# Performance work log

Measured on AMD Instinct MI355X. Metric: run time of the kernel, lower is better.

## Reference

```python
import jax, jax.numpy as jnp
import numpy as np

C = 1024          # columns
K = 16            # cells per column
S = 32            # distal segments per cell
Y = 128           # synapses per segment
N = C * K         # num cells
PERM_THR = 0.5
ACT_THR = 10
LR = 0.1          # volatile learning rate
MOD = 1.0         # modulation_signal


def setup_inputs() -> dict:
    key = jax.random.key(0)
    k1, k2, k3, k4, k5 = jax.random.split(key, 5)
    x = jax.random.uniform(k1, (C,)) < 0.03                      # sparse column SDR
    prev_active_cells = jax.random.uniform(k2, (N,)) < 0.12      # prev-step active cells
    distal_connections = jax.random.randint(k3, (N, S, Y), 0, N, dtype=jnp.int32)
    volatile_permanences = jax.random.uniform(k4, (N, S, Y), dtype=jnp.float32)
    consolidated_permanences = jax.random.uniform(k5, (N, S, Y), dtype=jnp.float32) * 0.6
    return {
        "x": x,
        "prev_active_cells": prev_active_cells,
        "distal_connections": distal_connections,
        "volatile_permanences": volatile_permanences,
        "consolidated_permanences": consolidated_permanences,
    }


def reference(x, prev_active_cells, distal_connections, volatile_permanences, consolidated_permanences):
    conn = jnp.clip(distal_connections, 0, N - 1)                # [N,S,Y]
    x_active = x.astype(bool)                                    # [C]
    prev_any = prev_active_cells.any()

    # ---- phase 1: predictive state per column from prev_active_cells ----
    presyn_prev = prev_active_cells[conn]                        # [N,S,Y] irregular gather
    connected = (volatile_permanences > PERM_THR) | (consolidated_permanences > PERM_THR)
    active_syn = (connected & presyn_prev).sum(-1)               # [N,S]
    pred_cell = (active_syn >= ACT_THR).any(-1)                  # [N]
    pred_col = pred_cell.reshape(C, K)                           # [C,K]
    col_predicted = pred_col.any(-1)                             # [C]

    # ---- burst winner selection (unthresholded overlaps, argmax over K*S) ----
    overlaps = presyn_prev.sum(-1).astype(jnp.int32)             # [N,S]
    best_flat = jnp.argmax(overlaps.reshape(C, K * S), axis=-1)  # [C]
    burst_winner_local = best_flat // S                          # [C] (== 0 when no prev activity, matching torch fallback)
    burst_winner_mask = jax.nn.one_hot(burst_winner_local, K, dtype=bool)  # [C,K]

    winner = jnp.where(col_predicted[:, None], pred_col, burst_winner_mask)  # [C,K]
    winner = winner & x_active[:, None]                          # only active columns

    # new active cells: only bursting columns set cells (predicted columns set none, per source)
    new_active = jnp.broadcast_to((x_active & ~col_predicted)[:, None], (C, K))
    new_active_flat = new_active.reshape(-1)                     # [N]

    # ---- learning: update volatile permanences on each winner cell's best segment ----
    best_seg = jnp.argmax(overlaps, axis=-1)                     # [N]
    rows = jnp.arange(N)
    presyn_best = presyn_prev[rows, best_seg]                    # [N,Y]
    old_row = volatile_permanences[rows, best_seg]               # [N,Y]
    pot = LR * MOD
    pun = pot * 0.1
    new_row = jnp.clip(old_row + jnp.where(presyn_best, pot, -pun), 0.0, 1.0)
    learn_mask = winner.reshape(-1) & prev_any                   # [N] (torch skips learning if no prev activity)
    vol_new = volatile_permanences.at[rows, best_seg].set(
        jnp.where(learn_mask[:, None], new_row, old_row))

    # ---- phase 2: predictive state for next step from new active cells + updated perms ----
    presyn_new = new_active_flat[conn]                           # [N,S,Y]
    connected2 = (vol_new > PERM_THR) | (consolidated_permanences > PERM_THR)
    pred_next = (((connected2 & presyn_new).sum(-1)) >= ACT_THR).any(-1)  # [N]

    num_active = x_active.sum()
    num_pred = (x_active & col_predicted).sum()
    acc = jnp.where(num_active > 0,
                    num_pred.astype(jnp.float32) / jnp.maximum(num_active, 1).astype(jnp.float32),
                    jnp.float32(1.0))
    return new_active_flat, pred_next, acc
```

## Files before the change

kernel.cpp:

```cpp
#include <hip/hip_runtime.h>
#include <stdint.h>

#define C_ 1024
#define K_ 16
#define S_ 32
#define Y_ 128
#define N_ (C_ * K_)
#define ACT_THR 10
#define PERM_THR 0.5f
#define POT 0.1f
#define PUN 0.01f

#define WS_NUM_ACTIVE 0
#define WS_NUM_PRED   1
#define WS_NBURST     2
#define WS_LEARN_CNT  3
#define WS_PREV_ANY   4
#define WS_BURSTMASK  8
#define WS_PREVMASK   64
#define WS_CELLINFO   1024
#define WS_LIST       (1024 + N_)
#define WS_CONBITS    65536


__global__ __launch_bounds__(512) void pack_kernel(const int* __restrict__ prev,
                                                   unsigned* __restrict__ ws) {
    const int tid = threadIdx.x;
    if (tid < 64) ws[tid] = 0u;
    __syncthreads();
    const int4* p = reinterpret_cast<const int4*>(prev + tid * 32);
    unsigned m = 0u;
    #pragma unroll
    for (int q = 0; q < 8; ++q) {
        const int4 v = p[q];
        m |= (v.x != 0 ? 1u : 0u) << (q * 4 + 0);
        m |= (v.y != 0 ? 1u : 0u) << (q * 4 + 1);
        m |= (v.z != 0 ? 1u : 0u) << (q * 4 + 2);
        m |= (v.w != 0 ? 1u : 0u) << (q * 4 + 3);
    }
    ws[WS_PREVMASK + tid] = m;
    const bool any = (__ballot(m != 0u) != 0ull);
    if ((tid & 63) == 0 && any) atomicOr(&ws[WS_PREV_ANY], 1u);
}

__global__ __launch_bounds__(256) void precompute_kernel(const float* __restrict__ vol,
                                                         const float* __restrict__ cons,
                                                         unsigned long long* __restrict__ conbits) {
    const int tid  = threadIdx.x;
    const int wave = tid >> 6;
    const int lane = tid & 63;
    const int half = lane >> 5;
    const int l32  = lane & 31;
    const int cell = blockIdx.x * 4 + wave;
    const size_t base = (size_t)cell * (S_ * Y_) + (size_t)half * Y_ + (size_t)(l32 * 4);

    float4 v0 = *reinterpret_cast<const float4*>(vol  + base);
    float4 s0 = *reinterpret_cast<const float4*>(cons + base);
    float4 v1 = *reinterpret_cast<const float4*>(vol  + base + 256);
    float4 s1 = *reinterpret_cast<const float4*>(cons + base + 256);

    unsigned long long bits = 0ull;
    #pragma unroll 4
    for (int i = 0; i < 16; ++i) {
        const float4 vv = v0, sv = s0;
        v0 = v1; s0 = s1;
        if (i < 14) {
            const size_t nb = base + (size_t)(i + 2) * 256;
            v1 = *reinterpret_cast<const float4*>(vol  + nb);
            s1 = *reinterpret_cast<const float4*>(cons + nb);
        }
        const unsigned nib = ((vv.x > PERM_THR || sv.x > PERM_THR) ? 1u : 0u)
                           | ((vv.y > PERM_THR || sv.y > PERM_THR) ? 2u : 0u)
                           | ((vv.z > PERM_THR || sv.z > PERM_THR) ? 4u : 0u)
                           | ((vv.w > PERM_THR || sv.w > PERM_THR) ? 8u : 0u);
        bits |= ((unsigned long long)nib) << (4 * i);
    }
    conbits[(size_t)cell * 64 + lane] = bits;
}

__global__ __launch_bounds__(256) void phase1b_kernel(const int* __restrict__ conn,
                                                      const unsigned long long* __restrict__ conbits,
                                                      unsigned* __restrict__ ws) {
    __shared__ unsigned prevmask[512];
    const int tid = threadIdx.x;
    for (int i = tid; i < 512; i += 256) prevmask[i] = ws[WS_PREVMASK + i];
    __syncthreads();

    const int wave = tid >> 6;
    const int lane = tid & 63;
    const int half = lane >> 5;
    const int l32  = lane & 31;
    const int sh   = half * 32;
    const int cell = blockIdx.x * 4 + wave;
    const size_t base = (size_t)cell * (S_ * Y_) + (size_t)half * Y_ + (size_t)(l32 * 4);

    unsigned long long bits = conbits[(size_t)cell * 64 + lane];
    int4 a0 = *reinterpret_cast<const int4*>(conn + base);
    int4 a1 = *reinterpret_cast<const int4*>(conn + base + 256);

    unsigned key = 0u;
    bool predf = false;

    #pragma unroll 4
    for (int i = 0; i < 16; ++i) {
        const int4 cv = a0;
        a0 = a1;
        if (i < 14) a1 = *reinterpret_cast<const int4*>(conn + base + (size_t)(i + 2) * 256);

        const unsigned nib = (unsigned)bits & 0xFu;
        bits >>= 4;

        const int m0 = min(max(cv.x, 0), N_ - 1);
        const int m1 = min(max(cv.y, 0), N_ - 1);
        const int m2 = min(max(cv.z, 0), N_ - 1);
        const int m3 = min(max(cv.w, 0), N_ - 1);
        const bool p0 = (prevmask[m0 >> 5] >> (m0 & 31)) & 1u;
        const bool p1 = (prevmask[m1 >> 5] >> (m1 & 31)) & 1u;
        const bool p2 = (prevmask[m2 >> 5] >> (m2 & 31)) & 1u;
        const bool p3 = (prevmask[m3 >> 5] >> (m3 & 31)) & 1u;
        const bool c0 = nib & 1u;
        const bool c1 = nib & 2u;
        const bool c2 = nib & 4u;
        const bool c3 = nib & 8u;

        const uint64_t bp0 = __ballot(p0), bp1 = __ballot(p1),
                       bp2 = __ballot(p2), bp3 = __ballot(p3);
        const uint64_t ba0 = __ballot(p0 && c0), ba1 = __ballot(p1 && c1),
                       ba2 = __ballot(p2 && c2), ba3 = __ballot(p3 && c3);

        const int ov = __popc((unsigned)(bp0 >> sh)) + __popc((unsigned)(bp1 >> sh)) +
                       __popc((unsigned)(bp2 >> sh)) + __popc((unsigned)(bp3 >> sh));
        const int ac = __popc((unsigned)(ba0 >> sh)) + __popc((unsigned)(ba1 >> sh)) +
                       __popc((unsigned)(ba2 >> sh)) + __popc((unsigned)(ba3 >> sh));

        predf |= (ac >= ACT_THR);
        const int seg = 2 * i + half;
        const unsigned k2 = ((unsigned)ov << 6) | (unsigned)(63 - seg);
        key = max(key, k2);
    }

    const unsigned okey = (unsigned)__shfl_xor((int)key, 32);
    const unsigned fkey = max(key, okey);
    const bool fpred = (__any(predf ? 1 : 0) != 0);
    if (lane == 0) {
        const int bo = (int)(fkey >> 6);
        const int bs = 63 - (int)(fkey & 63u);
        ws[WS_CELLINFO + cell] = (fpred ? 1u : 0u) | ((unsigned)bs << 8) | ((unsigned)bo << 16);
    }
}

__global__ __launch_bounds__(256) void column_kernel(const int* __restrict__ x,
                                                     unsigned*  __restrict__ ws,
                                                     float*     __restrict__ out_new_active) {
    const int c = blockIdx.x * 256 + threadIdx.x;
    if (c >= C_) return;
    const bool xa = (x[c] != 0);
    const int base = c * K_;

    unsigned info[K_];
    bool colpred = false;
    int bo = -1, bk = 0;
    #pragma unroll
    for (int k = 0; k < K_; ++k) {
        const unsigned inf = ws[WS_CELLINFO + base + k];
        info[k] = inf;
        if (inf & 1u) colpred = true;
        const int ov = (int)((inf >> 16) & 0xFFu);
        if (ov > bo) { bo = ov; bk = k; }
    }

    const bool burst = xa && !colpred;
    const float nav = burst ? 1.0f : 0.0f;
    #pragma unroll
    for (int k = 0; k < K_; ++k) out_new_active[base + k] = nav;

    if (xa) {
        atomicAdd(&ws[WS_NUM_ACTIVE], 1u);
        if (colpred) atomicAdd(&ws[WS_NUM_PRED], 1u);
    }
    if (burst) {
        atomicAdd(&ws[WS_NBURST], 1u);
        atomicOr(&ws[WS_BURSTMASK + (c >> 5)], 1u << (c & 31));
    }
    if (xa) {
        if (colpred) {
            #pragma unroll
            for (int k = 0; k < K_; ++k) {
                if (info[k] & 1u) {
                    const unsigned i = atomicAdd(&ws[WS_LEARN_CNT], 1u);
                    ws[WS_LIST + i] = (unsigned)(base + k);
                }
            }
        } else {
            const unsigned i = atomicAdd(&ws[WS_LEARN_CNT], 1u);
            ws[WS_LIST + i] = (unsigned)(base + bk);
        }
    }
}

__global__ __launch_bounds__(256) void learnb_kernel(const int*   __restrict__ conn,
                                                     float*       __restrict__ vol,
                                                     const float* __restrict__ cons,
                                                     unsigned*    __restrict__ ws,
                                                     float*       __restrict__ out_acc) {
    __shared__ unsigned prevmask[512];
    const int tid = threadIdx.x;
    for (int i = tid; i < 512; i += 256) prevmask[i] = ws[WS_PREVMASK + i];
    __syncthreads();

    if (blockIdx.x == 0 && tid == 0) {
        const int na  = (int)ws[WS_NUM_ACTIVE];
        const int np_ = (int)ws[WS_NUM_PRED];
        out_acc[0] = (na > 0) ? ((float)np_ / (float)na) : 1.0f;
    }
    if (ws[WS_PREV_ANY] == 0u) return;

    const int cnt = (int)ws[WS_LEARN_CNT];
    const int hw  = (blockIdx.x * 256 + tid) >> 5;
    const int g   = tid & 31;
    const int nhw = gridDim.x * 8;
    unsigned* conbits32 = ws + WS_CONBITS;

    for (int e = hw; e < cnt; e += nhw) {
        const int cellv = (int)ws[WS_LIST + e];
        const int seg   = (int)((ws[WS_CELLINFO + cellv] >> 8) & 0xFFu);
        const size_t base = ((size_t)cellv * S_ + seg) * Y_ + (size_t)(g * 4);
        const int4   cv = *reinterpret_cast<const int4*>(conn + base);
        float4       vv = *reinterpret_cast<float4*>(vol + base);
        const float4 sv = *reinterpret_cast<const float4*>(cons + base);
        const int m0 = min(max(cv.x, 0), N_ - 1);
        const int m1 = min(max(cv.y, 0), N_ - 1);
        const int m2 = min(max(cv.z, 0), N_ - 1);
        const int m3 = min(max(cv.w, 0), N_ - 1);
        const bool p0 = (prevmask[m0 >> 5] >> (m0 & 31)) & 1u;
        const bool p1 = (prevmask[m1 >> 5] >> (m1 & 31)) & 1u;
        const bool p2 = (prevmask[m2 >> 5] >> (m2 & 31)) & 1u;
        const bool p3 = (prevmask[m3 >> 5] >> (m3 & 31)) & 1u;
        vv.x = fminf(fmaxf(vv.x + (p0 ? POT : -PUN), 0.0f), 1.0f);
        vv.y = fminf(fmaxf(vv.y + (p1 ? POT : -PUN), 0.0f), 1.0f);
        vv.z = fminf(fmaxf(vv.z + (p2 ? POT : -PUN), 0.0f), 1.0f);
        vv.w = fminf(fmaxf(vv.w + (p3 ? POT : -PUN), 0.0f), 1.0f);
        *reinterpret_cast<float4*>(vol + base) = vv;

        const unsigned nib = ((vv.x > PERM_THR || sv.x > PERM_THR) ? 1u : 0u)
                           | ((vv.y > PERM_THR || sv.y > PERM_THR) ? 2u : 0u)
                           | ((vv.z > PERM_THR || sv.z > PERM_THR) ? 4u : 0u)
                           | ((vv.w > PERM_THR || sv.w > PERM_THR) ? 8u : 0u);
        const int chunk = seg >> 1;
        const int slot  = (seg & 1) * 32 + g;
        const unsigned idx = (unsigned)(cellv * 128 + slot * 2 + (chunk >> 3));
        const int shn = 4 * (chunk & 7);
        const unsigned old = conbits32[idx];
        conbits32[idx] = (old & ~(0xFu << shn)) | (nib << shn);
    }
}

__global__ __launch_bounds__(256) void phase2b_kernel(const int* __restrict__ conn,
                                                      const unsigned long long* __restrict__ conbits,
                                                      const unsigned* __restrict__ ws,
                                                      float* __restrict__ out_pred_next) {
    __shared__ unsigned nburst_s;
    __shared__ unsigned burstmask[32];
    const int tid = threadIdx.x;
    if (tid == 0) nburst_s = ws[WS_NBURST];
    if (tid >= 64 && tid < 96) burstmask[tid - 64] = ws[WS_BURSTMASK + (tid - 64)];
    __syncthreads();

    const int cbase = blockIdx.x * 4;
    if (nburst_s == 0u) {
        if (tid < 4) out_pred_next[cbase + tid] = 0.0f;
        return;
    }

    const int wave = tid >> 6;
    const int lane = tid & 63;
    const int half = lane >> 5;
    const int l32  = lane & 31;
    const int sh   = half * 32;
    const int cell = cbase + wave;
    const size_t base = (size_t)cell * (S_ * Y_) + (size_t)half * Y_ + (size_t)(l32 * 4);

    unsigned long long bits = conbits[(size_t)cell * 64 + lane];
    int4 a0 = *reinterpret_cast<const int4*>(conn + base);
    int4 a1 = *reinterpret_cast<const int4*>(conn + base + 256);

    bool predf = false;

    #pragma unroll 4
    for (int i = 0; i < 16; ++i) {
        const int4 cv = a0;
        a0 = a1;
        if (i < 14) a1 = *reinterpret_cast<const int4*>(conn + base + (size_t)(i + 2) * 256);

        const unsigned nib = (unsigned)bits & 0xFu;
        bits >>= 4;

        const int m0 = min(max(cv.x, 0), N_ - 1) >> 4;
        const int m1 = min(max(cv.y, 0), N_ - 1) >> 4;
        const int m2 = min(max(cv.z, 0), N_ - 1) >> 4;
        const int m3 = min(max(cv.w, 0), N_ - 1) >> 4;
        const bool p0 = (burstmask[m0 >> 5] >> (m0 & 31)) & 1u;
        const bool p1 = (burstmask[m1 >> 5] >> (m1 & 31)) & 1u;
        const bool p2 = (burstmask[m2 >> 5] >> (m2 & 31)) & 1u;
        const bool p3 = (burstmask[m3 >> 5] >> (m3 & 31)) & 1u;
        const bool c0 = nib & 1u;
        const bool c1 = nib & 2u;
        const bool c2 = nib & 4u;
        const bool c3 = nib & 8u;

        const uint64_t ba0 = __ballot(p0 && c0), ba1 = __ballot(p1 && c1),
                       ba2 = __ballot(p2 && c2), ba3 = __ballot(p3 && c3);
        const int ac = __popc((unsigned)(ba0 >> sh)) + __popc((unsigned)(ba1 >> sh)) +
                       __popc((unsigned)(ba2 >> sh)) + __popc((unsigned)(ba3 >> sh));
        predf |= (ac >= ACT_THR);
    }

    const bool fpred = (__any(predf ? 1 : 0) != 0);
    if (lane == 0) out_pred_next[cell] = fpred ? 1.0f : 0.0f;
}

__global__ __launch_bounds__(256) void phase1_old(const int*   __restrict__ conn,
                                                  const float* __restrict__ vol,
                                                  const float* __restrict__ cons,
                                                  unsigned*    __restrict__ ws) {
    __shared__ unsigned prevmask[512];
    const int tid = threadIdx.x;
    for (int i = tid; i < 512; i += 256) prevmask[i] = ws[WS_PREVMASK + i];
    __syncthreads();

    const int wave = tid >> 6;
    const int lane = tid & 63;
    const int half = lane >> 5;
    const int l32  = lane & 31;
    const int sh   = half * 32;

    #pragma unroll 1
    for (int ci = 0; ci < 2; ++ci) {
        const int cell = blockIdx.x * 8 + wave + ci * 4;
        const size_t cellbase = (size_t)cell * (S_ * Y_) + (size_t)(l32 * 4);

        size_t a = cellbase + (size_t)half * Y_;
        int4   cv_n = *reinterpret_cast<const int4*>(conn + a);
        float4 vv_n = *reinterpret_cast<const float4*>(vol + a);
        float4 sv_n = *reinterpret_cast<const float4*>(cons + a);

        unsigned key = 0u;
        bool predf = false;

        #pragma unroll 2
        for (int i = 0; i < 16; ++i) {
            const int4   cv = cv_n;
            const float4 vv = vv_n;
            const float4 sv = sv_n;
            if (i < 15) {
                const size_t nb = cellbase + (size_t)(2 * (i + 1) + half) * Y_;
                cv_n = *reinterpret_cast<const int4*>(conn + nb);
                vv_n = *reinterpret_cast<const float4*>(vol + nb);
                sv_n = *reinterpret_cast<const float4*>(cons + nb);
            }

            const int m0 = min(max(cv.x, 0), N_ - 1);
            const int m1 = min(max(cv.y, 0), N_ - 1);
            const int m2 = min(max(cv.z, 0), N_ - 1);
            const int m3 = min(max(cv.w, 0), N_ - 1);
            const bool p0 = (prevmask[m0 >> 5] >> (m0 & 31)) & 1u;
            const bool p1 = (prevmask[m1 >> 5] >> (m1 & 31)) & 1u;
            const bool p2 = (prevmask[m2 >> 5] >> (m2 & 31)) & 1u;
            const bool p3 = (prevmask[m3 >> 5] >> (m3 & 31)) & 1u;
            const bool c0 = (vv.x > PERM_THR) || (sv.x > PERM_THR);
            const bool c1 = (vv.y > PERM_THR) || (sv.y > PERM_THR);
            const bool c2 = (vv.z > PERM_THR) || (sv.z > PERM_THR);
            const bool c3 = (vv.w > PERM_THR) || (sv.w > PERM_THR);

            const uint64_t bp0 = __ballot(p0), bp1 = __ballot(p1),
                           bp2 = __ballot(p2), bp3 = __ballot(p3);
            const uint64_t ba0 = __ballot(p0 && c0), ba1 = __ballot(p1 && c1),
                           ba2 = __ballot(p2 && c2), ba3 = __ballot(p3 && c3);

            const int ov = __popc((unsigned)(bp0 >> sh)) + __popc((unsigned)(bp1 >> sh)) +
                           __popc((unsigned)(bp2 >> sh)) + __popc((unsigned)(bp3 >> sh));
            const int ac = __popc((unsigned)(ba0 >> sh)) + __popc((unsigned)(ba1 >> sh)) +
                           __popc((unsigned)(ba2 >> sh)) + __popc((unsigned)(ba3 >> sh));

            predf |= (ac >= ACT_THR);
            const int seg = 2 * i + half;
            const unsigned k2 = ((unsigned)ov << 6) | (unsigned)(63 - seg);
            key = max(key, k2);
        }

        const unsigned okey = (unsigned)__shfl_xor((int)key, 32);
        const unsigned fkey = max(key, okey);
        const bool fpred = (__any(predf ? 1 : 0) != 0);
        if (lane == 0) {
            const int bo = (int)(fkey >> 6);
            const int bs = 63 - (int)(fkey & 63u);
            ws[WS_CELLINFO + cell] = (fpred ? 1u : 0u) | ((unsigned)bs << 8) | ((unsigned)bo << 16);
        }
    }
}

__global__ __launch_bounds__(256) void learn_old(const int* __restrict__ conn,
                                                 float*     __restrict__ vol,
                                                 unsigned*  __restrict__ ws,
                                                 float*     __restrict__ out_acc) {
    __shared__ unsigned prevmask[512];
    const int tid = threadIdx.x;
    for (int i = tid; i < 512; i += 256) prevmask[i] = ws[WS_PREVMASK + i];
    __syncthreads();

    if (blockIdx.x == 0 && tid == 0) {
        const int na  = (int)ws[WS_NUM_ACTIVE];
        const int np_ = (int)ws[WS_NUM_PRED];
        out_acc[0] = (na > 0) ? ((float)np_ / (float)na) : 1.0f;
    }
    if (ws[WS_PREV_ANY] == 0u) return;

    const int cnt    = (int)ws[WS_LEARN_CNT];
    const int wave   = (blockIdx.x * 256 + tid) >> 6;
    const int lane   = tid & 63;
    const int nwaves = gridDim.x * 4;

    for (int e = wave; e < cnt; e += nwaves) {
        const int cell = (int)ws[WS_LIST + e];
        const int seg  = (int)((ws[WS_CELLINFO + cell] >> 8) & 0xFFu);
        const size_t base = ((size_t)cell * S_ + seg) * Y_ + (size_t)(lane * 2);
        const int2 cv = *reinterpret_cast<const int2*>(conn + base);
        float2 vv = *reinterpret_cast<const float2*>(vol + base);
        const int m0 = min(max(cv.x, 0), N_ - 1);
        const int m1 = min(max(cv.y, 0), N_ - 1);
        const bool p0 = (prevmask[m0 >> 5] >> (m0 & 31)) & 1u;
        const bool p1 = (prevmask[m1 >> 5] >> (m1 & 31)) & 1u;
        vv.x = fminf(fmaxf(vv.x + (p0 ? POT : -PUN), 0.0f), 1.0f);
        vv.y = fminf(fmaxf(vv.y + (p1 ? POT : -PUN), 0.0f), 1.0f);
        *reinterpret_cast<float2*>(vol + base) = vv;
    }
}

__global__ __launch_bounds__(256) void phase2_old(const int*   __restrict__ conn,
                                                  const float* __restrict__ vol,
                                                  const float* __restrict__ cons,
                                                  const unsigned* __restrict__ ws,
                                                  float* __restrict__ out_pred_next) {
    __shared__ unsigned nburst_s;
    __shared__ unsigned burstmask[32];
    const int tid = threadIdx.x;
    if (tid == 0) nburst_s = ws[WS_NBURST];
    if (tid >= 64 && tid < 96) burstmask[tid - 64] = ws[WS_BURSTMASK + (tid - 64)];
    __syncthreads();

    const int cbase = blockIdx.x * 8;
    if (nburst_s == 0u) {
        if (tid < 8) out_pred_next[cbase + tid] = 0.0f;
        return;
    }

    const int wave = tid >> 6;
    const int lane = tid & 63;
    const int half = lane >> 5;
    const int l32  = lane & 31;
    const int sh   = half * 32;

    #pragma unroll 1
    for (int ci = 0; ci < 2; ++ci) {
        const int cell = cbase + wave + ci * 4;
        const size_t cellbase = (size_t)cell * (S_ * Y_) + (size_t)(l32 * 4);

        size_t a = cellbase + (size_t)half * Y_;
        int4   cv_n = *reinterpret_cast<const int4*>(conn + a);
        float4 vv_n = *reinterpret_cast<const float4*>(vol + a);
        float4 sv_n = *reinterpret_cast<const float4*>(cons + a);

        bool predf = false;

        #pragma unroll 2
        for (int i = 0; i < 16; ++i) {
            const int4   cv = cv_n;
            const float4 vv = vv_n;
            const float4 sv = sv_n;
            if (i < 15) {
                const size_t nb = cellbase + (size_t)(2 * (i + 1) + half) * Y_;
                cv_n = *reinterpret_cast<const int4*>(conn + nb);
                vv_n = *reinterpret_cast<const float4*>(vol + nb);
                sv_n = *reinterpret_cast<const float4*>(cons + nb);
            }

            const int m0 = min(max(cv.x, 0), N_ - 1) >> 4;
            const int m1 = min(max(cv.y, 0), N_ - 1) >> 4;
            const int m2 = min(max(cv.z, 0), N_ - 1) >> 4;
            const int m3 = min(max(cv.w, 0), N_ - 1) >> 4;
            const bool p0 = (burstmask[m0 >> 5] >> (m0 & 31)) & 1u;
            const bool p1 = (burstmask[m1 >> 5] >> (m1 & 31)) & 1u;
            const bool p2 = (burstmask[m2 >> 5] >> (m2 & 31)) & 1u;
            const bool p3 = (burstmask[m3 >> 5] >> (m3 & 31)) & 1u;
            const bool c0 = (vv.x > PERM_THR) || (sv.x > PERM_THR);
            const bool c1 = (vv.y > PERM_THR) || (sv.y > PERM_THR);
            const bool c2 = (vv.z > PERM_THR) || (sv.z > PERM_THR);
            const bool c3 = (vv.w > PERM_THR) || (sv.w > PERM_THR);

            const uint64_t ba0 = __ballot(p0 && c0), ba1 = __ballot(p1 && c1),
                           ba2 = __ballot(p2 && c2), ba3 = __ballot(p3 && c3);
            const int ac = __popc((unsigned)(ba0 >> sh)) + __popc((unsigned)(ba1 >> sh)) +
                           __popc((unsigned)(ba2 >> sh)) + __popc((unsigned)(ba3 >> sh));
            predf |= (ac >= ACT_THR);
        }

        const bool fpred = (__any(predf ? 1 : 0) != 0);
        if (lane == 0) out_pred_next[cell] = fpred ? 1.0f : 0.0f;
    }
}

extern "C" void kernel_launch(void* const* d_in, const int* in_sizes, int n_in,
                              void* d_out, int out_size, void* d_ws, size_t ws_size,
                              hipStream_t stream) {
    const int*   x    = (const int*)d_in[0];
    const int*   prev = (const int*)d_in[1];
    const int*   conn = (const int*)d_in[2];
    float*       vol  = (float*)d_in[3];
    const float* cons = (const float*)d_in[4];
    float*    out = (float*)d_out;
    unsigned* ws  = (unsigned*)d_ws;

    const size_t need = (size_t)WS_CONBITS * 4 + (size_t)N_ * 64 * 8;

    pack_kernel<<<1, 512, 0, stream>>>(prev, ws);

    if (ws_size >= need) {
        unsigned long long* conbits = (unsigned long long*)(ws + WS_CONBITS);
        precompute_kernel<<<N_ / 4, 256, 0, stream>>>(vol, cons, conbits);
        phase1b_kernel   <<<N_ / 4, 256, 0, stream>>>(conn, conbits, ws);
        column_kernel    <<<C_ / 256, 256, 0, stream>>>(x, ws, out);
        learnb_kernel    <<<64, 256, 0, stream>>>(conn, vol, cons, ws, out + 2 * N_);
        phase2b_kernel   <<<N_ / 4, 256, 0, stream>>>(conn, conbits, ws, out + N_);
    } else {
        phase1_old<<<2048, 256, 0, stream>>>(conn, vol, cons, ws);
        column_kernel<<<C_ / 256, 256, 0, stream>>>(x, ws, out);
        learn_old<<<64, 256, 0, stream>>>(conn, vol, ws, out + 2 * N_);
        phase2_old<<<2048, 256, 0, stream>>>(conn, vol, cons, ws, out + N_);
    }
}
```

Before: 680.6 us.

## Fuse connectivity precompute into phase1 and process multiple cells per wave

Merges the separate precompute kernel, which built connected-synapse bitmasks from volatile and consolidated permanences, into the phase-1 kernel, so the bitmasks are computed while the connections are streamed instead of being written and read back in an extra launch. Each wave now handles two cells in phase 1 and four in phase 2 to raise memory-level parallelism, uses nontemporal loads for the permanence arrays, and reverses the phase-2 block order, presumably to hit L2 data still resident from learning. In exchange it needs more registers per thread and fewer blocks per launch, which could lower occupancy.

```diff
diff --git a/kernel.cpp b/kernel.cpp
--- a/kernel.cpp
+++ b/kernel.cpp
@@ -10,6 +10,9 @@
 #define PERM_THR 0.5f
 #define POT 0.1f
 #define PUN 0.01f
+
+typedef float f4 __attribute__((ext_vector_type(4)));
+typedef int   i4 __attribute__((ext_vector_type(4)));
 
 #define WS_NUM_ACTIVE 0
 #define WS_NUM_PRED   1
@@ -43,44 +46,11 @@
     if ((tid & 63) == 0 && any) atomicOr(&ws[WS_PREV_ANY], 1u);
 }
 
-__global__ __launch_bounds__(256) void precompute_kernel(const float* __restrict__ vol,
-                                                         const float* __restrict__ cons,
-                                                         unsigned long long* __restrict__ conbits) {
-    const int tid  = threadIdx.x;
-    const int wave = tid >> 6;
-    const int lane = tid & 63;
-    const int half = lane >> 5;
-    const int l32  = lane & 31;
-    const int cell = blockIdx.x * 4 + wave;
-    const size_t base = (size_t)cell * (S_ * Y_) + (size_t)half * Y_ + (size_t)(l32 * 4);
-
-    float4 v0 = *reinterpret_cast<const float4*>(vol  + base);
-    float4 s0 = *reinterpret_cast<const float4*>(cons + base);
-    float4 v1 = *reinterpret_cast<const float4*>(vol  + base + 256);
-    float4 s1 = *reinterpret_cast<const float4*>(cons + base + 256);
-
-    unsigned long long bits = 0ull;
-    #pragma unroll 4
-    for (int i = 0; i < 16; ++i) {
-        const float4 vv = v0, sv = s0;
-        v0 = v1; s0 = s1;
-        if (i < 14) {
-            const size_t nb = base + (size_t)(i + 2) * 256;
-            v1 = *reinterpret_cast<const float4*>(vol  + nb);
-            s1 = *reinterpret_cast<const float4*>(cons + nb);
-        }
-        const unsigned nib = ((vv.x > PERM_THR || sv.x > PERM_THR) ? 1u : 0u)
-                           | ((vv.y > PERM_THR || sv.y > PERM_THR) ? 2u : 0u)
-                           | ((vv.z > PERM_THR || sv.z > PERM_THR) ? 4u : 0u)
-                           | ((vv.w > PERM_THR || sv.w > PERM_THR) ? 8u : 0u);
-        bits |= ((unsigned long long)nib) << (4 * i);
-    }
-    conbits[(size_t)cell * 64 + lane] = bits;
-}
-
-__global__ __launch_bounds__(256) void phase1b_kernel(const int* __restrict__ conn,
-                                                      const unsigned long long* __restrict__ conbits,
-                                                      unsigned* __restrict__ ws) {
+__global__ __launch_bounds__(256) void phase1c_kernel(const int*   __restrict__ conn,
+                                                      const float* __restrict__ vol,
+                                                      const float* __restrict__ cons,
+                                                      unsigned long long* __restrict__ conbits,
+                                                      unsigned*    __restrict__ ws) {
     __shared__ unsigned prevmask[512];
     const int tid = threadIdx.x;
     for (int i = tid; i < 512; i += 256) prevmask[i] = ws[WS_PREVMASK + i];
@@ -91,42 +61,33 @@
     const int half = lane >> 5;
     const int l32  = lane & 31;
     const int sh   = half * 32;
-    const int cell = blockIdx.x * 4 + wave;
-    const size_t base = (size_t)cell * (S_ * Y_) + (size_t)half * Y_ + (size_t)(l32 * 4);
-
-    unsigned long long bits = conbits[(size_t)cell * 64 + lane];
-    int4 a0 = *reinterpret_cast<const int4*>(conn + base);
-    int4 a1 = *reinterpret_cast<const int4*>(conn + base + 256);
-
-    unsigned key = 0u;
-    bool predf = false;
-
-    #pragma unroll 4
-    for (int i = 0; i < 16; ++i) {
-        const int4 cv = a0;
-        a0 = a1;
-        if (i < 14) a1 = *reinterpret_cast<const int4*>(conn + base + (size_t)(i + 2) * 256);
-
-        const unsigned nib = (unsigned)bits & 0xFu;
-        bits >>= 4;
-
-        const int m0 = min(max(cv.x, 0), N_ - 1);
-        const int m1 = min(max(cv.y, 0), N_ - 1);
-        const int m2 = min(max(cv.z, 0), N_ - 1);
-        const int m3 = min(max(cv.w, 0), N_ - 1);
+
+    const int cellA = blockIdx.x * 8 + wave;
+    const int cellB = cellA + 4;
+    const size_t baseA = (size_t)cellA * (S_ * Y_) + (size_t)half * Y_ + (size_t)(l32 * 4);
+    const size_t baseB = (size_t)cellB * (S_ * Y_) + (size_t)half * Y_ + (size_t)(l32 * 4);
+
+    auto proc = [&](const i4 cv, const f4 vv, const f4 sv, const int i,
+                    unsigned& key, bool& predf, unsigned long long& bits) {
+        const unsigned nib = ((vv[0] > PERM_THR || sv[0] > PERM_THR) ? 1u : 0u)
+                           | ((vv[1] > PERM_THR || sv[1] > PERM_THR) ? 2u : 0u)
+                           | ((vv[2] > PERM_THR || sv[2] > PERM_THR) ? 4u : 0u)
+                           | ((vv[3] > PERM_THR || sv[3] > PERM_THR) ? 8u : 0u);
+        bits |= ((unsigned long long)nib) << (4 * i);
+
+        const int m0 = min(max(cv[0], 0), N_ - 1);
+        const int m1 = min(max(cv[1], 0), N_ - 1);
+        const int m2 = min(max(cv[2], 0), N_ - 1);
+        const int m3 = min(max(cv[3], 0), N_ - 1);
         const bool p0 = (prevmask[m0 >> 5] >> (m0 & 31)) & 1u;
         const bool p1 = (prevmask[m1 >> 5] >> (m1 & 31)) & 1u;
         const bool p2 = (prevmask[m2 >> 5] >> (m2 & 31)) & 1u;
         const bool p3 = (prevmask[m3 >> 5] >> (m3 & 31)) & 1u;
-        const bool c0 = nib & 1u;
-        const bool c1 = nib & 2u;
-        const bool c2 = nib & 4u;
-        const bool c3 = nib & 8u;
 
         const uint64_t bp0 = __ballot(p0), bp1 = __ballot(p1),
                        bp2 = __ballot(p2), bp3 = __ballot(p3);
-        const uint64_t ba0 = __ballot(p0 && c0), ba1 = __ballot(p1 && c1),
-                       ba2 = __ballot(p2 && c2), ba3 = __ballot(p3 && c3);
+        const uint64_t ba0 = __ballot(p0 && (nib & 1u)), ba1 = __ballot(p1 && (nib & 2u)),
+                       ba2 = __ballot(p2 && (nib & 4u)), ba3 = __ballot(p3 && (nib & 8u));
 
         const int ov = __popc((unsigned)(bp0 >> sh)) + __popc((unsigned)(bp1 >> sh)) +
                        __popc((unsigned)(bp2 >> sh)) + __popc((unsigned)(bp3 >> sh));
@@ -137,16 +98,49 @@
         const int seg = 2 * i + half;
         const unsigned k2 = ((unsigned)ov << 6) | (unsigned)(63 - seg);
         key = max(key, k2);
-    }
-
-    const unsigned okey = (unsigned)__shfl_xor((int)key, 32);
-    const unsigned fkey = max(key, okey);
-    const bool fpred = (__any(predf ? 1 : 0) != 0);
+    };
+
+    i4 cA = *reinterpret_cast<const i4*>(conn + baseA);
+    i4 cB = *reinterpret_cast<const i4*>(conn + baseB);
+    f4 vA = __builtin_nontemporal_load(reinterpret_cast<const f4*>(vol  + baseA));
+    f4 vB = __builtin_nontemporal_load(reinterpret_cast<const f4*>(vol  + baseB));
+    f4 sA = __builtin_nontemporal_load(reinterpret_cast<const f4*>(cons + baseA));
+    f4 sB = __builtin_nontemporal_load(reinterpret_cast<const f4*>(cons + baseB));
+
+    unsigned keyA = 0u, keyB = 0u;
+    bool pfA = false, pfB = false;
+    unsigned long long bitsA = 0ull, bitsB = 0ull;
+
+    #pragma unroll 3
+    for (int i = 0; i < 15; ++i) {
+        const size_t nA = baseA + (size_t)(i + 1) * 256;
+        const size_t nB = baseB + (size_t)(i + 1) * 256;
+        const i4 cA1 = *reinterpret_cast<const i4*>(conn + nA);
+        const i4 cB1 = *reinterpret_cast<const i4*>(conn + nB);
+        const f4 vA1 = __builtin_nontemporal_load(reinterpret_cast<const f4*>(vol  + nA));
+        const f4 vB1 = __builtin_nontemporal_load(reinterpret_cast<const f4*>(vol  + nB));
+        const f4 sA1 = __builtin_nontemporal_load(reinterpret_cast<const f4*>(cons + nA));
+        const f4 sB1 = __builtin_nontemporal_load(reinterpret_cast<const f4*>(cons + nB));
+
+        proc(cA, vA, sA, i, keyA, pfA, bitsA);
+        proc(cB, vB, sB, i, keyB, pfB, bitsB);
+
+        cA = cA1; vA = vA1; sA = sA1;
+        cB = cB1; vB = vB1; sB = sB1;
+    }
+    proc(cA, vA, sA, 15, keyA, pfA, bitsA);
+    proc(cB, vB, sB, 15, keyB, pfB, bitsB);
+
+    const unsigned fkA = max(keyA, (unsigned)__shfl_xor((int)keyA, 32));
+    const unsigned fkB = max(keyB, (unsigned)__shfl_xor((int)keyB, 32));
+    const bool fpA = (__any(pfA ? 1 : 0) != 0);
+    const bool fpB = (__any(pfB ? 1 : 0) != 0);
     if (lane == 0) {
-        const int bo = (int)(fkey >> 6);
-        const int bs = 63 - (int)(fkey & 63u);
-        ws[WS_CELLINFO + cell] = (fpred ? 1u : 0u) | ((unsigned)bs << 8) | ((unsigned)bo << 16);
-    }
+        ws[WS_CELLINFO + cellA] = (fpA ? 1u : 0u) | ((unsigned)(63 - (fkA & 63u)) << 8) | ((fkA >> 6) << 16);
+        ws[WS_CELLINFO + cellB] = (fpB ? 1u : 0u) | ((unsigned)(63 - (fkB & 63u)) << 8) | ((fkB >> 6) << 16);
+    }
+    conbits[(size_t)cellA * 64 + lane] = bitsA;
+    conbits[(size_t)cellB * 64 + lane] = bitsB;
 }
 
 __global__ __launch_bounds__(256) void column_kernel(const int* __restrict__ x,
@@ -255,7 +249,7 @@
     }
 }
 
-__global__ __launch_bounds__(256) void phase2b_kernel(const int* __restrict__ conn,
+__global__ __launch_bounds__(256) void phase2c_kernel(const int* __restrict__ conn,
                                                       const unsigned long long* __restrict__ conbits,
                                                       const unsigned* __restrict__ ws,
                                                       float* __restrict__ out_pred_next) {
@@ -266,9 +260,9 @@
     if (tid >= 64 && tid < 96) burstmask[tid - 64] = ws[WS_BURSTMASK + (tid - 64)];
     __syncthreads();
 
-    const int cbase = blockIdx.x * 4;
+    const int cbase = ((int)gridDim.x - 1 - (int)blockIdx.x) * 16;
     if (nburst_s == 0u) {
-        if (tid < 4) out_pred_next[cbase + tid] = 0.0f;
+        if (tid < 16) out_pred_next[cbase + tid] = 0.0f;
         return;
     }
 
@@ -277,46 +271,72 @@
     const int half = lane >> 5;
     const int l32  = lane & 31;
     const int sh   = half * 32;
-    const int cell = cbase + wave;
-    const size_t base = (size_t)cell * (S_ * Y_) + (size_t)half * Y_ + (size_t)(l32 * 4);
-
-    unsigned long long bits = conbits[(size_t)cell * 64 + lane];
-    int4 a0 = *reinterpret_cast<const int4*>(conn + base);
-    int4 a1 = *reinterpret_cast<const int4*>(conn + base + 256);
-
-    bool predf = false;
-
-    #pragma unroll 4
-    for (int i = 0; i < 16; ++i) {
-        const int4 cv = a0;
-        a0 = a1;
-        if (i < 14) a1 = *reinterpret_cast<const int4*>(conn + base + (size_t)(i + 2) * 256);
-
-        const unsigned nib = (unsigned)bits & 0xFu;
-        bits >>= 4;
-
-        const int m0 = min(max(cv.x, 0), N_ - 1) >> 4;
-        const int m1 = min(max(cv.y, 0), N_ - 1) >> 4;
-        const int m2 = min(max(cv.z, 0), N_ - 1) >> 4;
-        const int m3 = min(max(cv.w, 0), N_ - 1) >> 4;
+
+    const int c0i = cbase + wave;
+    const size_t off = (size_t)half * Y_ + (size_t)(l32 * 4);
+    const size_t b0 = (size_t)(c0i     ) * (S_ * Y_) + off;
+    const size_t b1 = (size_t)(c0i + 4 ) * (S_ * Y_) + off;
+    const size_t b2 = (size_t)(c0i + 8 ) * (S_ * Y_) + off;
+    const size_t b3 = (size_t)(c0i + 12) * (S_ * Y_) + off;
+
+    unsigned long long q0 = conbits[(size_t)(c0i     ) * 64 + lane];
+    unsigned long long q1 = conbits[(size_t)(c0i + 4 ) * 64 + lane];
+    unsigned long long q2 = conbits[(size_t)(c0i + 8 ) * 64 + lane];
+    unsigned long long q3 = conbits[(size_t)(c0i + 12) * 64 + lane];
+
+    auto proc = [&](const i4 cv, const unsigned nib, bool& predf) {
+        const int m0 = min(max(cv[0], 0), N_ - 1) >> 4;
+        const int m1 = min(max(cv[1], 0), N_ - 1) >> 4;
+        const int m2 = min(max(cv[2], 0), N_ - 1) >> 4;
+        const int m3 = min(max(cv[3], 0), N_ - 1) >> 4;
         const bool p0 = (burstmask[m0 >> 5] >> (m0 & 31)) & 1u;
         const bool p1 = (burstmask[m1 >> 5] >> (m1 & 31)) & 1u;
         const bool p2 = (burstmask[m2 >> 5] >> (m2 & 31)) & 1u;
         const bool p3 = (burstmask[m3 >> 5] >> (m3 & 31)) & 1u;
-        const bool c0 = nib & 1u;
-        const bool c1 = nib & 2u;
-        const bool c2 = nib & 4u;
-        const bool c3 = nib & 8u;
-
-        const uint64_t ba0 = __ballot(p0 && c0), ba1 = __ballot(p1 && c1),
-                       ba2 = __ballot(p2 && c2), ba3 = __ballot(p3 && c3);
+        const uint64_t ba0 = __ballot(p0 && (nib & 1u)), ba1 = __ballot(p1 && (nib & 2u)),
+                       ba2 = __ballot(p2 && (nib & 4u)), ba3 = __ballot(p3 && (nib & 8u));
         const int ac = __popc((unsigned)(ba0 >> sh)) + __popc((unsigned)(ba1 >> sh)) +
                        __popc((unsigned)(ba2 >> sh)) + __popc((unsigned)(ba3 >> sh));
         predf |= (ac >= ACT_THR);
-    }
-
-    const bool fpred = (__any(predf ? 1 : 0) != 0);
-    if (lane == 0) out_pred_next[cell] = fpred ? 1.0f : 0.0f;
+    };
+
+    i4 a0 = *reinterpret_cast<const i4*>(conn + b0);
+    i4 a1 = *reinterpret_cast<const i4*>(conn + b1);
+    i4 a2 = *reinterpret_cast<const i4*>(conn + b2);
+    i4 a3 = *reinterpret_cast<const i4*>(conn + b3);
+
+    bool f0 = false, f1 = false, f2 = false, f3 = false;
+
+    #pragma unroll 3
+    for (int i = 0; i < 15; ++i) {
+        const size_t d = (size_t)(i + 1) * 256;
+        const i4 n0 = *reinterpret_cast<const i4*>(conn + b0 + d);
+        const i4 n1 = *reinterpret_cast<const i4*>(conn + b1 + d);
+        const i4 n2 = *reinterpret_cast<const i4*>(conn + b2 + d);
+        const i4 n3 = *reinterpret_cast<const i4*>(conn + b3 + d);
+
+        proc(a0, (unsigned)q0 & 0xFu, f0); q0 >>= 4;
+        proc(a1, (unsigned)q1 & 0xFu, f1); q1 >>= 4;
+        proc(a2, (unsigned)q2 & 0xFu, f2); q2 >>= 4;
+        proc(a3, (unsigned)q3 & 0xFu, f3); q3 >>= 4;
+
+        a0 = n0; a1 = n1; a2 = n2; a3 = n3;
+    }
+    proc(a0, (unsigned)q0 & 0xFu, f0);
+    proc(a1, (unsigned)q1 & 0xFu, f1);
+    proc(a2, (unsigned)q2 & 0xFu, f2);
+    proc(a3, (unsigned)q3 & 0xFu, f3);
+
+    const bool g0 = (__any(f0 ? 1 : 0) != 0);
+    const bool g1 = (__any(f1 ? 1 : 0) != 0);
+    const bool g2 = (__any(f2 ? 1 : 0) != 0);
+    const bool g3 = (__any(f3 ? 1 : 0) != 0);
+    if (lane == 0) {
+        out_pred_next[c0i     ] = g0 ? 1.0f : 0.0f;
+        out_pred_next[c0i + 4 ] = g1 ? 1.0f : 0.0f;
+        out_pred_next[c0i + 8 ] = g2 ? 1.0f : 0.0f;
+        out_pred_next[c0i + 12] = g3 ? 1.0f : 0.0f;
+    }
 }
 
 __global__ __launch_bounds__(256) void phase1_old(const int*   __restrict__ conn,
@@ -526,11 +546,10 @@
 
     if (ws_size >= need) {
         unsigned long long* conbits = (unsigned long long*)(ws + WS_CONBITS);
-        precompute_kernel<<<N_ / 4, 256, 0, stream>>>(vol, cons, conbits);
-        phase1b_kernel   <<<N_ / 4, 256, 0, stream>>>(conn, conbits, ws);
-        column_kernel    <<<C_ / 256, 256, 0, stream>>>(x, ws, out);
-        learnb_kernel    <<<64, 256, 0, stream>>>(conn, vol, cons, ws, out + 2 * N_);
-        phase2b_kernel   <<<N_ / 4, 256, 0, stream>>>(conn, conbits, ws, out + N_);
+        phase1c_kernel<<<N_ / 8,  256, 0, stream>>>(conn, vol, cons, conbits, ws);
+        column_kernel <<<C_ / 256, 256, 0, stream>>>(x, ws, out);
+        learnb_kernel <<<64,      256, 0, stream>>>(conn, vol, cons, ws, out + 2 * N_);
+        phase2c_kernel<<<N_ / 16, 256, 0, stream>>>(conn, conbits, ws, out + N_);
     } else {
         phase1_old<<<2048, 256, 0, stream>>>(conn, vol, cons, ws);
         column_kernel<<<C_ / 256, 256, 0, stream>>>(x, ws, out);
```

New measurement: 667.5 us. About the same (-1.9%).
